# Kernel optimization log

Hardware: AMD Instinct MI355X
Metric: run time of the kernel (lower is better)

The kernel has to match this reference:

```python
import jax, jax.numpy as jnp
import numpy as np

SPATIAL_SHAPES = [(128, 128), (64, 64), (32, 32), (16, 16)]
D_MODEL = 256
N_HEADS = 8
N_LEVELS = 4
N_POINTS = 4
HEAD_DIM = D_MODEL // N_HEADS
B = 2
LEN_Q = sum(h * w for h, w in SPATIAL_SHAPES)  # 21760
LEN_IN = LEN_Q


def setup_inputs() -> dict:
    key = jax.random.key(0)
    ks = jax.random.split(key, 11)
    s = 1.0 / np.sqrt(D_MODEL).astype(np.float32)
    query = jax.random.normal(ks[0], (B, LEN_Q, D_MODEL), jnp.float32)
    reference_points = jax.random.uniform(ks[1], (B, LEN_Q, N_LEVELS, 2), jnp.float32)
    input_flatten = jax.random.normal(ks[2], (B, LEN_IN, D_MODEL), jnp.float32)
    W_off = jax.random.normal(ks[3], (D_MODEL, N_HEADS * N_LEVELS * N_POINTS * 2), jnp.float32) * s
    b_off = jnp.zeros((N_HEADS * N_LEVELS * N_POINTS * 2,), jnp.float32)
    W_attn = jax.random.normal(ks[4], (D_MODEL, N_HEADS * N_LEVELS * N_POINTS), jnp.float32) * s
    b_attn = jnp.zeros((N_HEADS * N_LEVELS * N_POINTS,), jnp.float32)
    W_val = jax.random.normal(ks[5], (D_MODEL, D_MODEL), jnp.float32) * s
    b_val = jnp.zeros((D_MODEL,), jnp.float32)
    W_out = jax.random.normal(ks[6], (D_MODEL, D_MODEL), jnp.float32) * s
    b_out = jnp.zeros((D_MODEL,), jnp.float32)
    return {"query": query, "reference_points": reference_points, "input_flatten": input_flatten,
            "W_off": W_off, "b_off": b_off, "W_attn": W_attn, "b_attn": b_attn,
            "W_val": W_val, "b_val": b_val, "W_out": W_out, "b_out": b_out}


def _ms_deform_core(value, sampling_locations, attention_weights):
    # value: (B, H, Dh, N_total); sampling_locations: (B, Lq, H, L, P, 2) in [0,1]
    # attention_weights: (B, Lq, H, L*P)
    Bv, Hn, Dh, _ = value.shape
    Lq = sampling_locations.shape[1]
    P = sampling_locations.shape[4]
    BN = Bv * Hn
    grids = 2.0 * sampling_locations - 1.0
    splits = np.cumsum([h * w for h, w in SPATIAL_SHAPES])[:-1].tolist()
    value_list = jnp.split(value, splits, axis=3)
    sampled_levels = []
    for lid, (Hh, Ww) in enumerate(SPATIAL_SHAPES):
        # (BN, H*W, Dh)
        val_flat = jnp.transpose(value_list[lid].reshape(BN, Dh, Hh * Ww), (0, 2, 1))
        # (BN, Lq, P, 2)
        g = jnp.transpose(grids[:, :, :, lid, :, :], (0, 2, 1, 3, 4)).reshape(BN, Lq, P, 2)
        ix = ((g[..., 0] + 1.0) * Ww - 1.0) / 2.0
        iy = ((g[..., 1] + 1.0) * Hh - 1.0) / 2.0
        ix0 = jnp.floor(ix).astype(jnp.int32)
        iy0 = jnp.floor(iy).astype(jnp.int32)
        ix1 = ix0 + 1
        iy1 = iy0 + 1
        fx = (ix - ix0.astype(ix.dtype))[..., None]
        fy = (iy - iy0.astype(iy.dtype))[..., None]

        def valid(yy, xx):
            return ((xx >= 0) & (xx < Ww) & (yy >= 0) & (yy < Hh)).astype(val_flat.dtype)[..., None]

        def gather(yy, xx):
            idx = (jnp.clip(yy, 0, Hh - 1) * Ww + jnp.clip(xx, 0, Ww - 1)).reshape(BN, Lq * P)
            out = jnp.take_along_axis(val_flat, idx[:, :, None], axis=1)
            return out.reshape(BN, Lq, P, Dh)

        v00 = gather(iy0, ix0) * valid(iy0, ix0)
        v01 = gather(iy0, ix1) * valid(iy0, ix1)
        v10 = gather(iy1, ix0) * valid(iy1, ix0)
        v11 = gather(iy1, ix1) * valid(iy1, ix1)
        sampled = ((1 - fx) * (1 - fy) * v00 + fx * (1 - fy) * v01
                   + (1 - fx) * fy * v10 + fx * fy * v11)  # (BN, Lq, P, Dh)
        sampled_levels.append(jnp.transpose(sampled, (0, 3, 1, 2)))  # (BN, Dh, Lq, P)
    # (BN, Dh, Lq, L*P)
    sv = jnp.stack(sampled_levels, axis=-2).reshape(BN, Dh, Lq, N_LEVELS * P)
    attn = jnp.transpose(attention_weights, (0, 2, 1, 3)).reshape(BN, 1, Lq, N_LEVELS * P)
    out = jnp.sum(sv * attn, axis=-1)  # (BN, Dh, Lq)
    out = out.reshape(Bv, Hn * Dh, Lq)
    return jnp.transpose(out, (0, 2, 1))  # (B, Lq, d_model)


def reference(query, reference_points, input_flatten, W_off, b_off, W_attn, b_attn, W_val, b_val, W_out, b_out):
    Bq, Lq, _ = query.shape
    Len_in = input_flatten.shape[1]
    value = input_flatten @ W_val + b_val  # (B, Len_in, d_model)
    offsets = (query @ W_off + b_off).reshape(Bq, Lq, N_HEADS, N_LEVELS, N_POINTS, 2)
    attn = jax.nn.softmax((query @ W_attn + b_attn).reshape(Bq, Lq, N_HEADS, N_LEVELS * N_POINTS), axis=-1)
    # normalizer is (W, H) per level
    offset_normalizer = jnp.asarray([[w, h] for h, w in SPATIAL_SHAPES], dtype=query.dtype)
    sampling_locations = (reference_points[:, :, None, :, None, :]
                          + offsets / offset_normalizer[None, None, None, :, None, :])
    value = jnp.transpose(value, (0, 2, 1)).reshape(Bq, N_HEADS, HEAD_DIM, Len_in)
    out = _ms_deform_core(value, sampling_locations, attn)
    return out @ W_out + b_out
```

## Files before the change

### kernel.cpp

```cpp
#include <hip/hip_runtime.h>
#include <hip/hip_bf16.h>
#include <hip/hip_fp16.h>
#include <type_traits>

#define B_    2
#define LQ_   21760
#define LEN_  21760
#define DM    256
#define NH    8
#define NL    4
#define NP    4
#define HD    32

#define WS_VAL   0u
#define WS_SAMP  22282240u
#define WS_OA    44564480u
#define WS_WT    77987840u

typedef __attribute__((ext_vector_type(4))) float f32x4;
typedef __attribute__((ext_vector_type(8))) short bf16x8;
typedef __attribute__((ext_vector_type(4))) unsigned int u32x4;
typedef __attribute__((ext_vector_type(2))) unsigned int u32x2;

__device__ __forceinline__ unsigned short f2bf(float v) {
    __hip_bfloat16 h = __float2bfloat16(v);
    return *reinterpret_cast<unsigned short*>(&h);
}
__device__ __forceinline__ unsigned int pk2bf(float a, float b) {
    return (unsigned int)f2bf(a) | ((unsigned int)f2bf(b) << 16);
}
__device__ __forceinline__ unsigned int pk2h(float a, float b) {
    __half2 h = __floats2half2_rn(a, b);
    union { __half2 h; unsigned int u; } c; c.h = h; return c.u;
}
__device__ __forceinline__ __half2 u2h2(unsigned int u) {
    union { unsigned int u; __half2 h; } c; c.u = u; return c.h;
}

__global__ __launch_bounds__(256) void wt_cvt_all(const float* __restrict__ Wv,
                                                  const float* __restrict__ Wo,
                                                  const float* __restrict__ Wa,
                                                  const float* __restrict__ Wu,
                                                  unsigned short* __restrict__ wt) {
    const float* Ws[4] = {Wv, Wo, Wa, Wu};
    const int Ns[4] = {256, 256, 128, 256};
    const unsigned int dof[4] = {0u, 65536u, 131072u, 163840u};
    const int m = blockIdx.z;
    const int n0 = blockIdx.x * 16, k0 = blockIdx.y * 16;
    if (n0 >= Ns[m]) return;
    __shared__ float tile[16][17];
    const int tx = threadIdx.x & 15, ty = threadIdx.x >> 4;
    tile[ty][tx] = Ws[m][(size_t)(k0 + ty) * Ns[m] + n0 + tx];
    __syncthreads();
    wt[dof[m] + (size_t)(n0 + ty) * 256 + k0 + tx] = f2bf(tile[tx][ty]);
}

template <bool AF32, typename TOut>
__global__ __launch_bounds__(256) void gemm_mfma(const void* __restrict__ Av,
                                                 const unsigned short* __restrict__ Bt,
                                                 const float* __restrict__ bias,
                                                 const float* __restrict__ bias2,
                                                 int nsplit,
                                                 TOut* __restrict__ C,
                                                 int M, int N, int K) {
    __shared__ unsigned short As[128 * 32];
    __shared__ unsigned short Bs[128 * 32];
    const int t = threadIdx.x;
    const int wv = t >> 6;
    const int ln = t & 63;
    const int m0 = blockIdx.x * 128;
    const int n0 = blockIdx.y * 128;
    const int wm = (wv & 1) * 64;
    const int wn = (wv >> 1) * 64;
    const int lrow = ln & 15;
    const int kq = ln >> 4;

    f32x4 acc[4][4] = {};

    for (int k0 = 0; k0 < K; k0 += 32) {
        if constexpr (AF32) {
            const float* Af = (const float*)Av;
#pragma unroll
            for (int c = 0; c < 4; ++c) {
                const int i = t + c * 256;
                const int row = i >> 3;
                const int kq4 = (i & 7) * 4;
                f32x4 v = *(const f32x4*)&Af[(size_t)(m0 + row) * K + k0 + kq4];
                uint2 p = make_uint2(pk2bf(v.x, v.y), pk2bf(v.z, v.w));
                *(uint2*)((char*)As + row * 64 + kq4 * 2) = p;
            }
#pragma unroll
            for (int c = 0; c < 2; ++c) {
                const int o = c * 4096 + t * 16;
                const int row = o >> 6;
                const int ke = (o & 63) >> 1;
                const unsigned short* gb = Bt + (size_t)(n0 + row) * K + k0 + ke;
                __builtin_amdgcn_global_load_lds(
                    (const __attribute__((address_space(1))) void*)gb,
                    (__attribute__((address_space(3))) void*)((char*)Bs + o), 16, 0, 0);
            }
        } else {
            const unsigned short* Ab = (const unsigned short*)Av;
#pragma unroll
            for (int c = 0; c < 2; ++c) {
                const int o = c * 4096 + t * 16;
                const int row = o >> 6;
                const int ke = (o & 63) >> 1;
                const unsigned short* ga = Ab + (size_t)(m0 + row) * K + k0 + ke;
                const unsigned short* gb = Bt + (size_t)(n0 + row) * K + k0 + ke;
                __builtin_amdgcn_global_load_lds(
                    (const __attribute__((address_space(1))) void*)ga,
                    (__attribute__((address_space(3))) void*)((char*)As + o), 16, 0, 0);
                __builtin_amdgcn_global_load_lds(
                    (const __attribute__((address_space(1))) void*)gb,
                    (__attribute__((address_space(3))) void*)((char*)Bs + o), 16, 0, 0);
            }
        }
        __syncthreads();

        bf16x8 af[4], bfr[4];
#pragma unroll
        for (int i = 0; i < 4; ++i) {
            af[i]  = *(const bf16x8*)((char*)As + (wm + i * 16 + lrow) * 64 + kq * 16);
            bfr[i] = *(const bf16x8*)((char*)Bs + (wn + i * 16 + lrow) * 64 + kq * 16);
        }
#pragma unroll
        for (int i = 0; i < 4; ++i)
#pragma unroll
            for (int j = 0; j < 4; ++j)
                acc[i][j] = __builtin_amdgcn_mfma_f32_16x16x32_bf16(af[i], bfr[j], acc[i][j], 0, 0, 0);
        __syncthreads();
    }

#pragma unroll
    for (int j = 0; j < 4; ++j) {
        const int n = n0 + wn + j * 16 + lrow;
        const float bb = (n < nsplit) ? bias[n] : bias2[n - nsplit];
#pragma unroll
        for (int i = 0; i < 4; ++i) {
            const int mrow = m0 + wm + i * 16 + kq * 4;
#pragma unroll
            for (int r = 0; r < 4; ++r) {
                const float v = acc[i][j][r] + bb;
                if constexpr (std::is_same<TOut, float>::value) {
                    C[(size_t)(mrow + r) * N + n] = v;
                } else if constexpr (std::is_same<TOut, __half>::value) {
                    C[(size_t)(mrow + r) * N + n] = __float2half(v);
                } else {
                    C[(size_t)(mrow + r) * N + n] = f2bf(v);
                }
            }
        }
    }
}

#define QB 8
__device__ __forceinline__ void accum4(const uint4& v, float w, float* acc) {
#pragma unroll
    for (int c = 0; c < 4; ++c) {
        const __half2 h = u2h2((&v.x)[c]);
        acc[c * 2]     = fmaf(w, __low2float(h),  acc[c * 2]);
        acc[c * 2 + 1] = fmaf(w, __high2float(h), acc[c * 2 + 1]);
    }
}

__global__ __launch_bounds__(256) void msda_sample4(const unsigned short* __restrict__ value,
                                                    const unsigned short* __restrict__ oa,
                                                    const float* __restrict__ refp,
                                                    unsigned short* __restrict__ samp) {
    __shared__ char smem[16384 + 256];
    unsigned int* s_pk = (unsigned int*)smem;
    float* s_off   = (float*)smem;
    float* s_logit = (float*)(smem + 8192);
    float* s_aw    = (float*)(smem + 12288);
    float* s_ref   = (float*)(smem + 16384);

    const int t = threadIdx.x;
    const int j = blockIdx.x;
    const int bq0 = ((j & 7) * 680 + (j >> 3)) * QB;
    const int b = bq0 / LQ_;

    {
        const unsigned short* oab = oa + (size_t)bq0 * 384;
        {
            const int ql = t >> 5, c = t & 31;
            u32x4 raw = __builtin_nontemporal_load((const u32x4*)(oab + (size_t)ql * 384) + c);
            float2 f0 = __half22float2(u2h2(raw.x));
            float2 f1 = __half22float2(u2h2(raw.y));
            float2 f2 = __half22float2(u2h2(raw.z));
            float2 f3 = __half22float2(u2h2(raw.w));
            f32x4 o0 = {f0.x, f0.y, f1.x, f1.y};
            f32x4 o1 = {f2.x, f2.y, f3.x, f3.y};
            ((f32x4*)s_off)[ql * 64 + c * 2] = o0;
            ((f32x4*)s_off)[ql * 64 + c * 2 + 1] = o1;
        }
        {
            const int ql = t >> 5, c = t & 31;
            u32x2 raw = __builtin_nontemporal_load((const u32x2*)(oab + (size_t)ql * 384 + 256) + c);
            float2 f0 = __half22float2(u2h2(raw.x));
            float2 f1 = __half22float2(u2h2(raw.y));
            f32x4 o0 = {f0.x, f0.y, f1.x, f1.y};
            ((f32x4*)s_logit)[ql * 32 + c] = o0;
        }
        if (t < 16)
            ((f32x4*)s_ref)[t] = __builtin_nontemporal_load((const f32x4*)(refp + (size_t)bq0 * 8) + t);
    }
    __syncthreads();

    if (t < 64) {
        const float* lg = s_logit + (t >> 3) * 128 + (t & 7) * 16;
        float m = -1e30f;
#pragma unroll
        for (int i = 0; i < 16; ++i) m = fmaxf(m, lg[i]);
        float e[16], s = 0.f;
#pragma unroll
        for (int i = 0; i < 16; ++i) { e[i] = __expf(lg[i] - m); s += e[i]; }
        const float inv = 1.f / s;
#pragma unroll
        for (int i = 0; i < 16; ++i) s_aw[t * 16 + i] = e[i] * inv;
    }
    __syncthreads();

    unsigned int pk0[4], pk1[4], pk2[4], pk3[4];
    {
        const int Wls[4] = {128, 64, 32, 16};
        const int Hls[4] = {128, 64, 32, 16};
        const int st_[4] = {0, 16384, 20480, 21504};
#pragma unroll
        for (int ii = 0; ii < 4; ++ii) {
            const int s = t * 4 + ii;
            const int q = s >> 7;
            const int rest = s & 127;
            const int h = rest >> 4;
            const int l = (rest >> 2) & 3;
            const int Wl = Wls[l], Hl = Hls[l], base = st_[l];
            const float ix = s_ref[q * 8 + l * 2]     * (float)Wl - 0.5f + s_off[q * 256 + rest * 2];
            const float iy = s_ref[q * 8 + l * 2 + 1] * (float)Hl - 0.5f + s_off[q * 256 + rest * 2 + 1];
            const float fix = floorf(ix), fiy = floorf(iy);
            const int x0 = (int)fix, y0 = (int)fiy;
            const int x1 = x0 + 1, y1 = y0 + 1;
            const float fx = ix - fix, fy = iy - fiy;
            const bool vx0 = (x0 >= 0) & (x0 < Wl);
            const bool vx1 = (x1 >= 0) & (x1 < Wl);
            const bool vy0 = (y0 >= 0) & (y0 < Hl);
            const bool vy1 = (y1 >= 0) & (y1 < Hl);
            const int cx0 = min(max(x0, 0), Wl - 1);
            const int cx1 = min(max(x1, 0), Wl - 1);
            const int cy0 = min(max(y0, 0), Hl - 1);
            const int cy1 = min(max(y1, 0), Hl - 1);
            const float aw = s_aw[(q * 8 + h) * 16 + (rest & 15)];
            const float w00 = aw * (1.f - fx) * (1.f - fy) * (float)(vx0 && vy0);
            const float w01 = aw * fx * (1.f - fy)         * (float)(vx1 && vy0);
            const float w10 = aw * (1.f - fx) * fy         * (float)(vx0 && vy1);
            const float w11 = aw * fx * fy                 * (float)(vx1 && vy1);
            pk0[ii] = (unsigned int)(base + cy0 * Wl + cx0) | ((unsigned int)(base + cy0 * Wl + cx1) << 16);
            pk1[ii] = (unsigned int)(base + cy1 * Wl + cx0) | ((unsigned int)(base + cy1 * Wl + cx1) << 16);
            pk2[ii] = pk2h(w00, w01);
            pk3[ii] = pk2h(w10, w11);
        }
    }
    __syncthreads();

#pragma unroll
    for (int ii = 0; ii < 4; ++ii) {
        const int s = t * 4 + ii;
        const int q = s >> 7;
        const int h = (s >> 4) & 7;
        const int swz = ((h & 3) << 2) ^ ((((h >> 2) ^ (q & 1)) & 1) << 4);
        *(uint4*)&s_pk[(s * 4) ^ swz] = make_uint4(pk0[ii], pk1[ii], pk2[ii], pk3[ii]);
    }
    __syncthreads();

    const int q = t >> 5;
    const int w = t & 31;
    const int h = w >> 2;
    const int dg = w & 3;
    const int swz = ((h & 3) << 2) ^ ((((h >> 2) ^ (q & 1)) & 1) << 4);
    const unsigned short* vbase = value + (size_t)b * LEN_ * DM + h * HD + dg * 8;

    float acc[8] = {0.f, 0.f, 0.f, 0.f, 0.f, 0.f, 0.f, 0.f};
    const int sbase = q * 128 + h * 16;
#pragma unroll
    for (int lp2 = 0; lp2 < 8; ++lp2) {
        const uint4 pkA = *(const uint4*)&s_pk[((sbase + 2 * lp2)     * 4) ^ swz];
        const uint4 pkB = *(const uint4*)&s_pk[((sbase + 2 * lp2 + 1) * 4) ^ swz];
        const uint4 a00 = *(const uint4*)(vbase + (size_t)(pkA.x & 0xffffu) * DM);
        const uint4 a01 = *(const uint4*)(vbase + (size_t)(pkA.x >> 16) * DM);
        const uint4 a10 = *(const uint4*)(vbase + (size_t)(pkA.y & 0xffffu) * DM);
        const uint4 a11 = *(const uint4*)(vbase + (size_t)(pkA.y >> 16) * DM);
        const uint4 b00 = *(const uint4*)(vbase + (size_t)(pkB.x & 0xffffu) * DM);
        const uint4 b01 = *(const uint4*)(vbase + (size_t)(pkB.x >> 16) * DM);
        const uint4 b10 = *(const uint4*)(vbase + (size_t)(pkB.y & 0xffffu) * DM);
        const uint4 b11 = *(const uint4*)(vbase + (size_t)(pkB.y >> 16) * DM);
        const __half2 wA0 = u2h2(pkA.z), wA1 = u2h2(pkA.w);
        const __half2 wB0 = u2h2(pkB.z), wB1 = u2h2(pkB.w);
        accum4(a00, __low2float(wA0),  acc);
        accum4(a01, __high2float(wA0), acc);
        accum4(a10, __low2float(wA1),  acc);
        accum4(a11, __high2float(wA1), acc);
        accum4(b00, __low2float(wB0),  acc);
        accum4(b01, __high2float(wB0), acc);
        accum4(b10, __low2float(wB1),  acc);
        accum4(b11, __high2float(wB1), acc);
    }
    u32x4 o;
    o.x = pk2bf(acc[0], acc[1]);
    o.y = pk2bf(acc[2], acc[3]);
    o.z = pk2bf(acc[4], acc[5]);
    o.w = pk2bf(acc[6], acc[7]);
    __builtin_nontemporal_store(o, (u32x4*)(samp + (size_t)(bq0 + q) * 256 + h * HD + dg * 8));
}

extern "C" void kernel_launch(void* const* d_in, const int* in_sizes, int n_in,
                              void* d_out, int out_size, void* d_ws, size_t ws_size,
                              hipStream_t stream) {
    const float* query  = (const float*)d_in[0];
    const float* refp   = (const float*)d_in[1];
    const float* inpf   = (const float*)d_in[2];
    const float* W_off  = (const float*)d_in[3];
    const float* b_off  = (const float*)d_in[4];
    const float* W_attn = (const float*)d_in[5];
    const float* b_attn = (const float*)d_in[6];
    const float* W_val  = (const float*)d_in[7];
    const float* b_val  = (const float*)d_in[8];
    const float* W_out  = (const float*)d_in[9];
    const float* b_out  = (const float*)d_in[10];
    float* out = (float*)d_out;

    char* ws = (char*)d_ws;
    unsigned short* val_h  = (unsigned short*)(ws + WS_VAL);
    unsigned short* samp_bf = (unsigned short*)(ws + WS_SAMP);
    unsigned short* oa_h   = (unsigned short*)(ws + WS_OA);
    unsigned short* wt     = (unsigned short*)(ws + WS_WT);
    unsigned short* Wt_val = wt;
    unsigned short* Wt_oa  = wt + 65536;
    unsigned short* Wt_out = wt + 163840;

    const int M = B_ * LQ_;

    wt_cvt_all<<<dim3(16, 16, 4), 256, 0, stream>>>(W_val, W_off, W_attn, W_out, wt);

    gemm_mfma<true, __half><<<dim3(M / 128, 2), 256, 0, stream>>>(
        inpf, Wt_val, b_val, b_val, 256, (__half*)val_h, M, 256, 256);
    gemm_mfma<true, __half><<<dim3(M / 128, 3), 256, 0, stream>>>(
        query, Wt_oa, b_off, b_attn, 256, (__half*)oa_h, M, 384, 256);

    msda_sample4<<<dim3(M / QB), 256, 0, stream>>>(val_h, oa_h, refp, samp_bf);

    gemm_mfma<false, float><<<dim3(M / 128, 2), 256, 0, stream>>>(
        samp_bf, Wt_out, b_out, b_out, 256, out, M, 256, 256);
}
```

Measured before the change: 296.5 us.

## Store value per-head, merge pre-GEMMs, restructure sampler to paired-x taps

The value projection now writes its output in a head-major layout (b, head, pixel, 32), so each sampled pixel's head slice is a contiguous 64-byte row. The two input GEMMs are merged into one launch, and the grid is transposed so N-blocks sharing an M tile run adjacently. The sampler uses 4 queries per block with 64 threads per query. Each bilinear tap pair along x is fetched as one contiguous 16-element load split across two 8-lane halves, followed by a shuffle reduction. The aim is better gather locality and fewer index and weight entries, at the cost of scattered 2-byte stores in the GEMM epilogue and extra edge-case logic.

Result: faster. 290.1 us (-2.2%).

```diff
diff --git a/kernel.cpp b/kernel.cpp
--- a/kernel.cpp
+++ b/kernel.cpp
@@ -55,21 +55,26 @@
     wt[dof[m] + (size_t)(n0 + ty) * 256 + k0 + tx] = f2bf(tile[tx][ty]);
 }
 
-template <bool AF32, typename TOut>
-__global__ __launch_bounds__(256) void gemm_mfma(const void* __restrict__ Av,
-                                                 const unsigned short* __restrict__ Bt,
-                                                 const float* __restrict__ bias,
-                                                 const float* __restrict__ bias2,
-                                                 int nsplit,
-                                                 TOut* __restrict__ C,
-                                                 int M, int N, int K) {
+__global__ __launch_bounds__(256) void gemm_pre(const float* __restrict__ inpf,
+                                                const float* __restrict__ query,
+                                                const unsigned short* __restrict__ Wt_val,
+                                                const unsigned short* __restrict__ Wt_oa,
+                                                const float* __restrict__ b_val,
+                                                const float* __restrict__ b_off,
+                                                const float* __restrict__ b_attn,
+                                                unsigned short* __restrict__ val_h,
+                                                unsigned short* __restrict__ oa_h) {
     __shared__ unsigned short As[128 * 32];
     __shared__ unsigned short Bs[128 * 32];
     const int t = threadIdx.x;
     const int wv = t >> 6;
     const int ln = t & 63;
-    const int m0 = blockIdx.x * 128;
-    const int n0 = blockIdx.y * 128;
+    const int job = (blockIdx.x >= 2);
+    const int n0 = (job ? (blockIdx.x - 2) : blockIdx.x) * 128;
+    const int m0 = blockIdx.y * 128;
+    const float* A = job ? query : inpf;
+    const unsigned short* Bt = job ? Wt_oa : Wt_val;
+    const int K = 256;
     const int wm = (wv & 1) * 64;
     const int wn = (wv >> 1) * 64;
     const int lrow = ln & 15;
@@ -78,43 +83,24 @@
     f32x4 acc[4][4] = {};
 
     for (int k0 = 0; k0 < K; k0 += 32) {
-        if constexpr (AF32) {
-            const float* Af = (const float*)Av;
-#pragma unroll
-            for (int c = 0; c < 4; ++c) {
-                const int i = t + c * 256;
-                const int row = i >> 3;
-                const int kq4 = (i & 7) * 4;
-                f32x4 v = *(const f32x4*)&Af[(size_t)(m0 + row) * K + k0 + kq4];
-                uint2 p = make_uint2(pk2bf(v.x, v.y), pk2bf(v.z, v.w));
-                *(uint2*)((char*)As + row * 64 + kq4 * 2) = p;
-            }
-#pragma unroll
-            for (int c = 0; c < 2; ++c) {
-                const int o = c * 4096 + t * 16;
-                const int row = o >> 6;
-                const int ke = (o & 63) >> 1;
-                const unsigned short* gb = Bt + (size_t)(n0 + row) * K + k0 + ke;
-                __builtin_amdgcn_global_load_lds(
-                    (const __attribute__((address_space(1))) void*)gb,
-                    (__attribute__((address_space(3))) void*)((char*)Bs + o), 16, 0, 0);
-            }
-        } else {
-            const unsigned short* Ab = (const unsigned short*)Av;
-#pragma unroll
-            for (int c = 0; c < 2; ++c) {
-                const int o = c * 4096 + t * 16;
-                const int row = o >> 6;
-                const int ke = (o & 63) >> 1;
-                const unsigned short* ga = Ab + (size_t)(m0 + row) * K + k0 + ke;
-                const unsigned short* gb = Bt + (size_t)(n0 + row) * K + k0 + ke;
-                __builtin_amdgcn_global_load_lds(
-                    (const __attribute__((address_space(1))) void*)ga,
-                    (__attribute__((address_space(3))) void*)((char*)As + o), 16, 0, 0);
-                __builtin_amdgcn_global_load_lds(
-                    (const __attribute__((address_space(1))) void*)gb,
-                    (__attribute__((address_space(3))) void*)((char*)Bs + o), 16, 0, 0);
-            }
+#pragma unroll
+        for (int c = 0; c < 4; ++c) {
+            const int i = t + c * 256;
+            const int row = i >> 3;
+            const int kq4 = (i & 7) * 4;
+            f32x4 v = *(const f32x4*)&A[(size_t)(m0 + row) * K + k0 + kq4];
+            uint2 p = make_uint2(pk2bf(v.x, v.y), pk2bf(v.z, v.w));
+            *(uint2*)((char*)As + row * 64 + kq4 * 2) = p;
+        }
+#pragma unroll
+        for (int c = 0; c < 2; ++c) {
+            const int o = c * 4096 + t * 16;
+            const int row = o >> 6;
+            const int ke = (o & 63) >> 1;
+            const unsigned short* gb = Bt + (size_t)(n0 + row) * K + k0 + ke;
+            __builtin_amdgcn_global_load_lds(
+                (const __attribute__((address_space(1))) void*)gb,
+                (__attribute__((address_space(3))) void*)((char*)Bs + o), 16, 0, 0);
         }
         __syncthreads();
 
@@ -132,29 +118,95 @@
         __syncthreads();
     }
 
+    const int b = m0 / LQ_;
 #pragma unroll
     for (int j = 0; j < 4; ++j) {
         const int n = n0 + wn + j * 16 + lrow;
-        const float bb = (n < nsplit) ? bias[n] : bias2[n - nsplit];
+        const float bb = job ? ((n < 256) ? b_off[n] : b_attn[n - 256]) : b_val[n];
 #pragma unroll
         for (int i = 0; i < 4; ++i) {
             const int mrow = m0 + wm + i * 16 + kq * 4;
 #pragma unroll
             for (int r = 0; r < 4; ++r) {
                 const float v = acc[i][j][r] + bb;
-                if constexpr (std::is_same<TOut, float>::value) {
-                    C[(size_t)(mrow + r) * N + n] = v;
-                } else if constexpr (std::is_same<TOut, __half>::value) {
-                    C[(size_t)(mrow + r) * N + n] = __float2half(v);
+                const unsigned short hv = (unsigned short)__half_as_ushort(__float2half(v));
+                if (job) {
+                    oa_h[(size_t)(mrow + r) * 384 + n] = hv;
                 } else {
-                    C[(size_t)(mrow + r) * N + n] = f2bf(v);
+                    const int pix = (mrow + r) - b * LQ_;
+                    const int h = n >> 5, c = n & 31;
+                    val_h[((size_t)(b * NH + h) * LQ_ + pix) * HD + c] = hv;
                 }
             }
         }
     }
 }
 
-#define QB 8
+__global__ __launch_bounds__(256) void gemm_out(const unsigned short* __restrict__ Ab,
+                                                const unsigned short* __restrict__ Bt,
+                                                const float* __restrict__ bias,
+                                                float* __restrict__ C) {
+    __shared__ unsigned short As[128 * 32];
+    __shared__ unsigned short Bs[128 * 32];
+    const int t = threadIdx.x;
+    const int wv = t >> 6;
+    const int ln = t & 63;
+    const int n0 = blockIdx.x * 128;
+    const int m0 = blockIdx.y * 128;
+    const int N = 256, K = 256;
+    const int wm = (wv & 1) * 64;
+    const int wn = (wv >> 1) * 64;
+    const int lrow = ln & 15;
+    const int kq = ln >> 4;
+
+    f32x4 acc[4][4] = {};
+
+    for (int k0 = 0; k0 < K; k0 += 32) {
+#pragma unroll
+        for (int c = 0; c < 2; ++c) {
+            const int o = c * 4096 + t * 16;
+            const int row = o >> 6;
+            const int ke = (o & 63) >> 1;
+            const unsigned short* ga = Ab + (size_t)(m0 + row) * K + k0 + ke;
+            const unsigned short* gb = Bt + (size_t)(n0 + row) * K + k0 + ke;
+            __builtin_amdgcn_global_load_lds(
+                (const __attribute__((address_space(1))) void*)ga,
+                (__attribute__((address_space(3))) void*)((char*)As + o), 16, 0, 0);
+            __builtin_amdgcn_global_load_lds(
+                (const __attribute__((address_space(1))) void*)gb,
+                (__attribute__((address_space(3))) void*)((char*)Bs + o), 16, 0, 0);
+        }
+        __syncthreads();
+
+        bf16x8 af[4], bfr[4];
+#pragma unroll
+        for (int i = 0; i < 4; ++i) {
+            af[i]  = *(const bf16x8*)((char*)As + (wm + i * 16 + lrow) * 64 + kq * 16);
+            bfr[i] = *(const bf16x8*)((char*)Bs + (wn + i * 16 + lrow) * 64 + kq * 16);
+        }
+#pragma unroll
+        for (int i = 0; i < 4; ++i)
+#pragma unroll
+            for (int j = 0; j < 4; ++j)
+                acc[i][j] = __builtin_amdgcn_mfma_f32_16x16x32_bf16(af[i], bfr[j], acc[i][j], 0, 0, 0);
+        __syncthreads();
+    }
+
+#pragma unroll
+    for (int j = 0; j < 4; ++j) {
+        const int n = n0 + wn + j * 16 + lrow;
+        const float bb = bias[n];
+#pragma unroll
+        for (int i = 0; i < 4; ++i) {
+            const int mrow = m0 + wm + i * 16 + kq * 4;
+#pragma unroll
+            for (int r = 0; r < 4; ++r)
+                C[(size_t)(mrow + r) * N + n] = acc[i][j][r] + bb;
+        }
+    }
+}
+
+#define QB 4
 __device__ __forceinline__ void accum4(const uint4& v, float w, float* acc) {
 #pragma unroll
     for (int c = 0; c < 4; ++c) {
@@ -164,50 +216,39 @@
     }
 }
 
-__global__ __launch_bounds__(256) void msda_sample4(const unsigned short* __restrict__ value,
+__global__ __launch_bounds__(256) void msda_sample5(const unsigned short* __restrict__ value,
                                                     const unsigned short* __restrict__ oa,
                                                     const float* __restrict__ refp,
                                                     unsigned short* __restrict__ samp) {
-    __shared__ char smem[16384 + 256];
-    unsigned int* s_pk = (unsigned int*)smem;
+    __shared__ char smem[8320];
+    unsigned int* s_pkw = (unsigned int*)smem;
     float* s_off   = (float*)smem;
-    float* s_logit = (float*)(smem + 8192);
-    float* s_aw    = (float*)(smem + 12288);
-    float* s_ref   = (float*)(smem + 16384);
+    float* s_logit = (float*)(smem + 4096);
+    float* s_aw    = (float*)(smem + 6144);
+    float* s_ref   = (float*)(smem + 8192);
 
     const int t = threadIdx.x;
     const int j = blockIdx.x;
-    const int bq0 = ((j & 7) * 680 + (j >> 3)) * QB;
+    const int bq0 = ((j & 7) * 1360 + (j >> 3)) * QB;
     const int b = bq0 / LQ_;
 
     {
         const unsigned short* oab = oa + (size_t)bq0 * 384;
-        {
-            const int ql = t >> 5, c = t & 31;
-            u32x4 raw = __builtin_nontemporal_load((const u32x4*)(oab + (size_t)ql * 384) + c);
-            float2 f0 = __half22float2(u2h2(raw.x));
-            float2 f1 = __half22float2(u2h2(raw.y));
-            float2 f2 = __half22float2(u2h2(raw.z));
-            float2 f3 = __half22float2(u2h2(raw.w));
-            f32x4 o0 = {f0.x, f0.y, f1.x, f1.y};
-            f32x4 o1 = {f2.x, f2.y, f3.x, f3.y};
-            ((f32x4*)s_off)[ql * 64 + c * 2] = o0;
-            ((f32x4*)s_off)[ql * 64 + c * 2 + 1] = o1;
-        }
-        {
-            const int ql = t >> 5, c = t & 31;
-            u32x2 raw = __builtin_nontemporal_load((const u32x2*)(oab + (size_t)ql * 384 + 256) + c);
-            float2 f0 = __half22float2(u2h2(raw.x));
-            float2 f1 = __half22float2(u2h2(raw.y));
-            f32x4 o0 = {f0.x, f0.y, f1.x, f1.y};
-            ((f32x4*)s_logit)[ql * 32 + c] = o0;
-        }
-        if (t < 16)
+        const int q = t >> 6, c = t & 63;
+        u32x2 r0 = __builtin_nontemporal_load((const u32x2*)(oab + (size_t)q * 384) + c);
+        float2 f0 = __half22float2(u2h2(r0.x));
+        float2 f1 = __half22float2(u2h2(r0.y));
+        f32x4 o0 = {f0.x, f0.y, f1.x, f1.y};
+        ((f32x4*)s_off)[q * 64 + c] = o0;
+        unsigned int r1 = __builtin_nontemporal_load((const unsigned int*)(oab + (size_t)q * 384 + 256) + c);
+        float2 g0 = __half22float2(u2h2(r1));
+        ((float2*)s_logit)[q * 64 + c] = make_float2(g0.x, g0.y);
+        if (t < 8)
             ((f32x4*)s_ref)[t] = __builtin_nontemporal_load((const f32x4*)(refp + (size_t)bq0 * 8) + t);
     }
     __syncthreads();
 
-    if (t < 64) {
+    if (t < 32) {
         const float* lg = s_logit + (t >> 3) * 128 + (t & 7) * 16;
         float m = -1e30f;
 #pragma unroll
@@ -221,94 +262,78 @@
     }
     __syncthreads();
 
-    unsigned int pk0[4], pk1[4], pk2[4], pk3[4];
+    uint4 ent[2];
+    int wrd[2];
     {
         const int Wls[4] = {128, 64, 32, 16};
         const int Hls[4] = {128, 64, 32, 16};
         const int st_[4] = {0, 16384, 20480, 21504};
 #pragma unroll
-        for (int ii = 0; ii < 4; ++ii) {
-            const int s = t * 4 + ii;
+        for (int ii = 0; ii < 2; ++ii) {
+            const int s = t * 2 + ii;
             const int q = s >> 7;
             const int rest = s & 127;
             const int h = rest >> 4;
-            const int l = (rest >> 2) & 3;
+            const int lp = rest & 15;
+            const int l = lp >> 2;
             const int Wl = Wls[l], Hl = Hls[l], base = st_[l];
             const float ix = s_ref[q * 8 + l * 2]     * (float)Wl - 0.5f + s_off[q * 256 + rest * 2];
             const float iy = s_ref[q * 8 + l * 2 + 1] * (float)Hl - 0.5f + s_off[q * 256 + rest * 2 + 1];
             const float fix = floorf(ix), fiy = floorf(iy);
             const int x0 = (int)fix, y0 = (int)fiy;
-            const int x1 = x0 + 1, y1 = y0 + 1;
             const float fx = ix - fix, fy = iy - fiy;
-            const bool vx0 = (x0 >= 0) & (x0 < Wl);
-            const bool vx1 = (x1 >= 0) & (x1 < Wl);
-            const bool vy0 = (y0 >= 0) & (y0 < Hl);
-            const bool vy1 = (y1 >= 0) & (y1 < Hl);
-            const int cx0 = min(max(x0, 0), Wl - 1);
-            const int cx1 = min(max(x1, 0), Wl - 1);
+            int sx; float wl, wr;
+            if (x0 < 0)            { sx = 0;      wl = (x0 == -1) ? fx : 0.f;        wr = 0.f; }
+            else if (x0 >= Wl - 1) { sx = Wl - 2; wl = 0.f; wr = (x0 == Wl - 1) ? (1.f - fx) : 0.f; }
+            else                   { sx = x0;     wl = 1.f - fx;                     wr = fx; }
+            const float g0 = ((y0 >= 0) & (y0 < Hl)) ? (1.f - fy) : 0.f;
+            const float g1 = ((y0 + 1 >= 0) & (y0 + 1 < Hl)) ? fy : 0.f;
             const int cy0 = min(max(y0, 0), Hl - 1);
-            const int cy1 = min(max(y1, 0), Hl - 1);
-            const float aw = s_aw[(q * 8 + h) * 16 + (rest & 15)];
-            const float w00 = aw * (1.f - fx) * (1.f - fy) * (float)(vx0 && vy0);
-            const float w01 = aw * fx * (1.f - fy)         * (float)(vx1 && vy0);
-            const float w10 = aw * (1.f - fx) * fy         * (float)(vx0 && vy1);
-            const float w11 = aw * fx * fy                 * (float)(vx1 && vy1);
-            pk0[ii] = (unsigned int)(base + cy0 * Wl + cx0) | ((unsigned int)(base + cy0 * Wl + cx1) << 16);
-            pk1[ii] = (unsigned int)(base + cy1 * Wl + cx0) | ((unsigned int)(base + cy1 * Wl + cx1) << 16);
-            pk2[ii] = pk2h(w00, w01);
-            pk3[ii] = pk2h(w10, w11);
-        }
-    }
-    __syncthreads();
-
-#pragma unroll
-    for (int ii = 0; ii < 4; ++ii) {
-        const int s = t * 4 + ii;
-        const int q = s >> 7;
-        const int h = (s >> 4) & 7;
-        const int swz = ((h & 3) << 2) ^ ((((h >> 2) ^ (q & 1)) & 1) << 4);
-        *(uint4*)&s_pk[(s * 4) ^ swz] = make_uint4(pk0[ii], pk1[ii], pk2[ii], pk3[ii]);
-    }
-    __syncthreads();
-
-    const int q = t >> 5;
-    const int w = t & 31;
-    const int h = w >> 2;
-    const int dg = w & 3;
-    const int swz = ((h & 3) << 2) ^ ((((h >> 2) ^ (q & 1)) & 1) << 4);
-    const unsigned short* vbase = value + (size_t)b * LEN_ * DM + h * HD + dg * 8;
+            const int cy1 = min(max(y0 + 1, 0), Hl - 1);
+            const float aw = s_aw[(q * 8 + h) * 16 + lp];
+            ent[ii].x = (unsigned int)(base + cy0 * Wl + sx);
+            ent[ii].y = (unsigned int)(base + cy1 * Wl + sx);
+            ent[ii].z = pk2h(aw * wl * g0, aw * wr * g0);
+            ent[ii].w = pk2h(aw * wl * g1, aw * wr * g1);
+            wrd[ii] = q * 512 + lp * 32 + (((h ^ (lp & 7))) << 2);
+        }
+    }
+    __syncthreads();
+
+#pragma unroll
+    for (int ii = 0; ii < 2; ++ii)
+        *(uint4*)&s_pkw[wrd[ii]] = ent[ii];
+    __syncthreads();
+
+    const int q = t >> 6;
+    const int lane = t & 63;
+    const int h = lane >> 3;
+    const int dg = lane & 7;
+    const unsigned short* vb = value + ((size_t)(b * NH + h) * LQ_) * HD + dg * 8;
 
     float acc[8] = {0.f, 0.f, 0.f, 0.f, 0.f, 0.f, 0.f, 0.f};
-    const int sbase = q * 128 + h * 16;
-#pragma unroll
-    for (int lp2 = 0; lp2 < 8; ++lp2) {
-        const uint4 pkA = *(const uint4*)&s_pk[((sbase + 2 * lp2)     * 4) ^ swz];
-        const uint4 pkB = *(const uint4*)&s_pk[((sbase + 2 * lp2 + 1) * 4) ^ swz];
-        const uint4 a00 = *(const uint4*)(vbase + (size_t)(pkA.x & 0xffffu) * DM);
-        const uint4 a01 = *(const uint4*)(vbase + (size_t)(pkA.x >> 16) * DM);
-        const uint4 a10 = *(const uint4*)(vbase + (size_t)(pkA.y & 0xffffu) * DM);
-        const uint4 a11 = *(const uint4*)(vbase + (size_t)(pkA.y >> 16) * DM);
-        const uint4 b00 = *(const uint4*)(vbase + (size_t)(pkB.x & 0xffffu) * DM);
-        const uint4 b01 = *(const uint4*)(vbase + (size_t)(pkB.x >> 16) * DM);
-        const uint4 b10 = *(const uint4*)(vbase + (size_t)(pkB.y & 0xffffu) * DM);
-        const uint4 b11 = *(const uint4*)(vbase + (size_t)(pkB.y >> 16) * DM);
-        const __half2 wA0 = u2h2(pkA.z), wA1 = u2h2(pkA.w);
-        const __half2 wB0 = u2h2(pkB.z), wB1 = u2h2(pkB.w);
-        accum4(a00, __low2float(wA0),  acc);
-        accum4(a01, __high2float(wA0), acc);
-        accum4(a10, __low2float(wA1),  acc);
-        accum4(a11, __high2float(wA1), acc);
-        accum4(b00, __low2float(wB0),  acc);
-        accum4(b01, __high2float(wB0), acc);
-        accum4(b10, __low2float(wB1),  acc);
-        accum4(b11, __high2float(wB1), acc);
-    }
-    u32x4 o;
-    o.x = pk2bf(acc[0], acc[1]);
-    o.y = pk2bf(acc[2], acc[3]);
-    o.z = pk2bf(acc[4], acc[5]);
-    o.w = pk2bf(acc[6], acc[7]);
-    __builtin_nontemporal_store(o, (u32x4*)(samp + (size_t)(bq0 + q) * 256 + h * HD + dg * 8));
+#pragma unroll
+    for (int lp = 0; lp < 16; ++lp) {
+        const uint4 pk = *(const uint4*)&s_pkw[q * 512 + lp * 32 + ((h ^ (lp & 7)) << 2)];
+        const uint4 v0 = *(const uint4*)(vb + (size_t)pk.x * HD);
+        const uint4 v1 = *(const uint4*)(vb + (size_t)pk.y * HD);
+        const __half2 w0 = u2h2(pk.z), w1 = u2h2(pk.w);
+        const float f0 = (dg < 4) ? __low2float(w0) : __high2float(w0);
+        const float f1 = (dg < 4) ? __low2float(w1) : __high2float(w1);
+        accum4(v0, f0, acc);
+        accum4(v1, f1, acc);
+    }
+#pragma unroll
+    for (int i = 0; i < 8; ++i) acc[i] += __shfl_xor(acc[i], 4);
+
+    if (dg < 4) {
+        u32x4 o;
+        o.x = pk2bf(acc[0], acc[1]);
+        o.y = pk2bf(acc[2], acc[3]);
+        o.z = pk2bf(acc[4], acc[5]);
+        o.w = pk2bf(acc[6], acc[7]);
+        __builtin_nontemporal_store(o, (u32x4*)(samp + (size_t)(bq0 + q) * 256 + h * HD + dg * 8));
+    }
 }
 
 extern "C" void kernel_launch(void* const* d_in, const int* in_sizes, int n_in,
@@ -328,25 +353,22 @@
     float* out = (float*)d_out;
 
     char* ws = (char*)d_ws;
-    unsigned short* val_h  = (unsigned short*)(ws + WS_VAL);
+    unsigned short* val_h   = (unsigned short*)(ws + WS_VAL);
     unsigned short* samp_bf = (unsigned short*)(ws + WS_SAMP);
-    unsigned short* oa_h   = (unsigned short*)(ws + WS_OA);
-    unsigned short* wt     = (unsigned short*)(ws + WS_WT);
-    unsigned short* Wt_val = wt;
-    unsigned short* Wt_oa  = wt + 65536;
-    unsigned short* Wt_out = wt + 163840;
+    unsigned short* oa_h    = (unsigned short*)(ws + WS_OA);
+    unsigned short* wt      = (unsigned short*)(ws + WS_WT);
+    unsigned short* Wt_val  = wt;
+    unsigned short* Wt_oa   = wt + 65536;
+    unsigned short* Wt_out  = wt + 163840;
 
     const int M = B_ * LQ_;
 
     wt_cvt_all<<<dim3(16, 16, 4), 256, 0, stream>>>(W_val, W_off, W_attn, W_out, wt);
 
-    gemm_mfma<true, __half><<<dim3(M / 128, 2), 256, 0, stream>>>(
-        inpf, Wt_val, b_val, b_val, 256, (__half*)val_h, M, 256, 256);
-    gemm_mfma<true, __half><<<dim3(M / 128, 3), 256, 0, stream>>>(
-        query, Wt_oa, b_off, b_attn, 256, (__half*)oa_h, M, 384, 256);
-
-    msda_sample4<<<dim3(M / QB), 256, 0, stream>>>(val_h, oa_h, refp, samp_bf);
-
-    gemm_mfma<false, float><<<dim3(M / 128, 2), 256, 0, stream>>>(
-        samp_bf, Wt_out, b_out, b_out, 256, out, M, 256, 256);
-}
+    gemm_pre<<<dim3(5, M / 128), 256, 0, stream>>>(
+        inpf, query, Wt_val, Wt_oa, b_val, b_off, b_attn, val_h, oa_h);
+
+    msda_sample5<<<dim3(M / QB), 256, 0, stream>>>(val_h, oa_h, refp, samp_bf);
+
+    gemm_out<<<dim3(2, M / 128), 256, 0, stream>>>(samp_bf, Wt_out, b_out, out);
+}
```
